# Kernel tuning notes

Measured on AMD Instinct MI355X. Metric: run time of the kernel, lower is better.

## Reference

```python
import jax, jax.numpy as jnp
import numpy as np

B, S, D, H = 2, 2048, 1024, 16
HD = D // H  # head_dim = 64


def setup_inputs() -> dict:
    key = jax.random.key(0)
    ks = jax.random.split(key, 11)
    s = 1.0 / np.sqrt(D)
    return {
        "query": jax.random.normal(ks[0], (B, S, D), jnp.float32),
        "key": jax.random.normal(ks[1], (B, S, D), jnp.float32),
        "value": jax.random.normal(ks[2], (B, S, D), jnp.float32),
        "Wq": jax.random.uniform(ks[3], (D, D), jnp.float32, -s, s),
        "bq": jax.random.uniform(ks[4], (D,), jnp.float32, -s, s),
        "Wk": jax.random.uniform(ks[5], (D, D), jnp.float32, -s, s),
        "bk": jax.random.uniform(ks[6], (D,), jnp.float32, -s, s),
        "Wv": jax.random.uniform(ks[7], (D, D), jnp.float32, -s, s),
        "bv": jax.random.uniform(ks[8], (D,), jnp.float32, -s, s),
        "Wo": jax.random.uniform(ks[9], (D, D), jnp.float32, -s, s),
        "bo": jax.random.uniform(ks[10], (D,), jnp.float32, -s, s),
    }


def reference(query, key, value, Wq, bq, Wk, bk, Wv, bv, Wo, bo):
    # Linear projections (W stored as [in, out])
    q = query @ Wq + bq  # [B,S,D]
    k = key @ Wk + bk
    v = value @ Wv + bv
    # split heads -> [B,H,S,HD]
    q = q.reshape(B, S, H, HD).transpose(0, 2, 1, 3)
    k = k.reshape(B, S, H, HD).transpose(0, 2, 1, 3)
    v = v.reshape(B, S, H, HD).transpose(0, 2, 1, 3)
    scale = 1.0 / jnp.sqrt(jnp.float32(HD))
    scores = jnp.einsum("bhqd,bhkd->bhqk", q, k) * scale  # [B,H,S,S]
    attn = jax.nn.softmax(scores, axis=-1)
    out = jnp.einsum("bhqk,bhkd->bhqd", attn, v)  # [B,H,S,HD]
    out = out.transpose(0, 2, 1, 3).reshape(B, S, D)
    out = out @ Wo + bo
    return out, attn
```

## Files before the change

### kernel.cpp

```cpp
#include <hip/hip_runtime.h>

typedef __bf16 bf16;
typedef __bf16 bf16x8 __attribute__((ext_vector_type(8)));
typedef __bf16 bf16x4 __attribute__((ext_vector_type(4)));
typedef float  f32x4  __attribute__((ext_vector_type(4)));

#define B_ 2
#define S_ 2048
#define D_ 1024
#define H_ 16
#define HD_ 64
#define MROWS_ (B_*S_)

__global__ __launch_bounds__(256) void convert_kernel(
    const float* __restrict__ q, const float* __restrict__ k, const float* __restrict__ v,
    bf16* __restrict__ qx, bf16* __restrict__ kx, bf16* __restrict__ vx)
{
    size_t i = ((size_t)blockIdx.x * 256 + threadIdx.x) * 4;
    float4 a = *(const float4*)(q + i);
    float4 b = *(const float4*)(k + i);
    float4 c = *(const float4*)(v + i);
    bf16x4 oa = { (bf16)a.x, (bf16)a.y, (bf16)a.z, (bf16)a.w };
    bf16x4 ob = { (bf16)b.x, (bf16)b.y, (bf16)b.z, (bf16)b.w };
    bf16x4 oc = { (bf16)c.x, (bf16)c.y, (bf16)c.z, (bf16)c.w };
    *(bf16x4*)(qx + i) = oa;
    *(bf16x4*)(kx + i) = ob;
    *(bf16x4*)(vx + i) = oc;
}

__global__ __launch_bounds__(256) void wtrans_kernel(
    const float* __restrict__ W0, const float* __restrict__ W1,
    const float* __restrict__ W2, const float* __restrict__ W3,
    bf16* __restrict__ T0, bf16* __restrict__ T1,
    bf16* __restrict__ T2, bf16* __restrict__ T3)
{
    int z = blockIdx.z;
    const float* W = z == 0 ? W0 : (z == 1 ? W1 : (z == 2 ? W2 : W3));
    bf16* T = z == 0 ? T0 : (z == 1 ? T1 : (z == 2 ? T2 : T3));
    __shared__ float tile[32][33];
    int n0 = blockIdx.x * 32, k0 = blockIdx.y * 32;
    int tx = threadIdx.x, ty = threadIdx.y;
#pragma unroll
    for (int r = 0; r < 4; r++)
        tile[ty + r * 8][tx] = W[(size_t)(k0 + ty + r * 8) * D_ + n0 + tx];
    __syncthreads();
#pragma unroll
    for (int r = 0; r < 4; r++)
        T[(size_t)(n0 + ty + r * 8) * D_ + k0 + tx] = (bf16)tile[tx][ty + r * 8];
}

template <int OUT_MODE>
__global__ __launch_bounds__(256) void gemm_bias_kernel(
    const bf16* __restrict__ A0, const bf16* __restrict__ A1, const bf16* __restrict__ A2,
    const bf16* __restrict__ B0, const bf16* __restrict__ B1, const bf16* __restrict__ B2,
    const float* __restrict__ bias0, const float* __restrict__ bias1, const float* __restrict__ bias2,
    void* __restrict__ out0, void* __restrict__ out1, void* __restrict__ out2)
{
    constexpr int K = 1024, N = 1024;
    int z = blockIdx.z;
    const bf16* A = z == 0 ? A0 : (z == 1 ? A1 : A2);
    const bf16* Bt = z == 0 ? B0 : (z == 1 ? B1 : B2);
    const float* bias = z == 0 ? bias0 : (z == 1 ? bias1 : bias2);
    void* out = z == 0 ? out0 : (z == 1 ? out1 : out2);

    __shared__ bf16 sA[128][40];
    __shared__ bf16 sB[128][40];

    int tid = threadIdx.x, wave = tid >> 6, lane = tid & 63;
    int lrow = lane & 15, quad = lane >> 4;
    int m0 = blockIdx.y * 128, n0 = blockIdx.x * 128;
    int rb = (wave & 1) * 64, cb = (wave >> 1) * 64;

    f32x4 acc[4][4] = {};

    for (int k0 = 0; k0 < K; k0 += 32) {
        __syncthreads();
#pragma unroll
        for (int it = 0; it < 2; it++) {
            int idx = tid + it * 256;
            int r = idx >> 2, c = (idx & 3) * 8;
            *(uint4*)&sA[r][c] = *(const uint4*)(A + (size_t)(m0 + r) * K + k0 + c);
            *(uint4*)&sB[r][c] = *(const uint4*)(Bt + (size_t)(n0 + r) * K + k0 + c);
        }
        __syncthreads();
        bf16x8 af[4], bfv[4];
#pragma unroll
        for (int t = 0; t < 4; t++) {
            af[t]  = *(const bf16x8*)&sA[rb + t * 16 + lrow][quad * 8];
            bfv[t] = *(const bf16x8*)&sB[cb + t * 16 + lrow][quad * 8];
        }
#pragma unroll
        for (int rt = 0; rt < 4; rt++)
#pragma unroll
            for (int ct = 0; ct < 4; ct++)
                acc[rt][ct] = __builtin_amdgcn_mfma_f32_16x16x32_bf16(af[rt], bfv[ct], acc[rt][ct], 0, 0, 0);
    }

#pragma unroll
    for (int ct = 0; ct < 4; ct++) {
        int n = n0 + cb + ct * 16 + lrow;
        float bv = bias[n];
#pragma unroll
        for (int rt = 0; rt < 4; rt++) {
            int m = m0 + rb + rt * 16 + quad * 4;
#pragma unroll
            for (int rr = 0; rr < 4; rr++) {
                float val = acc[rt][ct][rr] + bv;
                if (OUT_MODE == 0) ((bf16*)out)[(size_t)(m + rr) * N + n] = (bf16)val;
                else               ((float*)out)[(size_t)(m + rr) * N + n] = val;
            }
        }
    }
}

__global__ __launch_bounds__(256) void vtrans_kernel(
    const bf16* __restrict__ vp, bf16* __restrict__ vT)
{
    __shared__ bf16 tile[64][72];
    int s0 = blockIdx.x * 64;
    int bh = blockIdx.y;
    int b = bh >> 4, h = bh & 15;
    int tid = threadIdx.x;
#pragma unroll
    for (int it = 0; it < 2; it++) {
        int idx = tid + it * 256;
        int s = idx >> 3, c = (idx & 7) * 8;
        *(uint4*)&tile[s][c] = *(const uint4*)&vp[(size_t)(b * S_ + s0 + s) * D_ + h * HD_ + c];
    }
    __syncthreads();
#pragma unroll
    for (int it = 0; it < 2; it++) {
        int idx = tid + it * 256;
        int d = idx >> 3, c = (idx & 7) * 8;
        bf16x8 t;
#pragma unroll
        for (int j = 0; j < 8; j++) t[j] = tile[c + j][d];
        *(bf16x8*)&vT[(size_t)(bh * HD_ + d) * S_ + s0 + c] = t;
    }
}

__global__ __launch_bounds__(256) void attn_kernel(
    const bf16* __restrict__ qp, const bf16* __restrict__ kp, const bf16* __restrict__ vT,
    float* __restrict__ attn, bf16* __restrict__ op)
{
    __shared__ bf16 sQ[64][72];
    __shared__ bf16 sK[128][72];
    __shared__ bf16 sVT[64][136];
    __shared__ bf16 sP[64][136];
    __shared__ float sInv[64];

    int qt = blockIdx.x, bh = blockIdx.y;
    int b = bh >> 4, h = bh & 15;
    int q0 = qt * 64;
    int tid = threadIdx.x, wave = tid >> 6, lane = tid & 63;
    int lrow = lane & 15, quad = lane >> 4;
    const float scale = 0.125f;

    const size_t qbase = (size_t)(b * S_ + q0) * D_ + h * HD_;
#pragma unroll
    for (int it = 0; it < 2; it++) {
        int idx = tid + it * 256;
        int r = idx >> 3, c = (idx & 7) * 8;
        *(uint4*)&sQ[r][c] = *(const uint4*)&qp[qbase + (size_t)r * D_ + c];
    }
    __syncthreads();
    bf16x8 aq0 = *(const bf16x8*)&sQ[wave * 16 + lrow][quad * 8];
    bf16x8 aq1 = *(const bf16x8*)&sQ[wave * 16 + lrow][32 + quad * 8];

    const size_t kbase0 = (size_t)(b * S_) * D_ + h * HD_;

    float rsum[4] = {0.f, 0.f, 0.f, 0.f};
    for (int kt = 0; kt < 16; kt++) {
        __syncthreads();
#pragma unroll
        for (int it = 0; it < 4; it++) {
            int idx = tid + it * 256;
            int r = idx >> 3, c = (idx & 7) * 8;
            *(uint4*)&sK[r][c] = *(const uint4*)&kp[kbase0 + (size_t)(kt * 128 + r) * D_ + c];
        }
        __syncthreads();
#pragma unroll
        for (int ct = 0; ct < 8; ct++) {
            f32x4 s = {0.f, 0.f, 0.f, 0.f};
            bf16x8 b0 = *(const bf16x8*)&sK[ct * 16 + lrow][quad * 8];
            bf16x8 b1 = *(const bf16x8*)&sK[ct * 16 + lrow][32 + quad * 8];
            s = __builtin_amdgcn_mfma_f32_16x16x32_bf16(aq0, b0, s, 0, 0, 0);
            s = __builtin_amdgcn_mfma_f32_16x16x32_bf16(aq1, b1, s, 0, 0, 0);
#pragma unroll
            for (int r = 0; r < 4; r++) rsum[r] += __expf(s[r] * scale);
        }
    }
#pragma unroll
    for (int off = 1; off < 16; off <<= 1)
#pragma unroll
        for (int r = 0; r < 4; r++) rsum[r] += __shfl_xor(rsum[r], off);
    if (lrow == 0) {
#pragma unroll
        for (int r = 0; r < 4; r++) sInv[wave * 16 + quad * 4 + r] = 1.0f / rsum[r];
    }
    __syncthreads();
    float inv[4];
#pragma unroll
    for (int r = 0; r < 4; r++) inv[r] = sInv[wave * 16 + quad * 4 + r];

    f32x4 oacc[4] = {};
    float* attn_base = attn + ((size_t)bh * S_ + q0) * S_;
    const size_t vbase = (size_t)(bh * HD_) * S_;
    for (int kt = 0; kt < 16; kt++) {
        __syncthreads();
#pragma unroll
        for (int it = 0; it < 4; it++) {
            int idx = tid + it * 256;
            int r = idx >> 3, c = (idx & 7) * 8;
            *(uint4*)&sK[r][c] = *(const uint4*)&kp[kbase0 + (size_t)(kt * 128 + r) * D_ + c];
        }
#pragma unroll
        for (int it = 0; it < 4; it++) {
            int idx = tid + it * 256;
            int d = idx >> 4, c = (idx & 15) * 8;
            *(uint4*)&sVT[d][c] = *(const uint4*)&vT[vbase + (size_t)d * S_ + kt * 128 + c];
        }
        __syncthreads();
#pragma unroll
        for (int ct = 0; ct < 8; ct++) {
            f32x4 s = {0.f, 0.f, 0.f, 0.f};
            bf16x8 b0 = *(const bf16x8*)&sK[ct * 16 + lrow][quad * 8];
            bf16x8 b1 = *(const bf16x8*)&sK[ct * 16 + lrow][32 + quad * 8];
            s = __builtin_amdgcn_mfma_f32_16x16x32_bf16(aq0, b0, s, 0, 0, 0);
            s = __builtin_amdgcn_mfma_f32_16x16x32_bf16(aq1, b1, s, 0, 0, 0);
            int key_local = ct * 16 + lrow;
#pragma unroll
            for (int r = 0; r < 4; r++) {
                float e = __expf(s[r] * scale) * inv[r];
                int qrow = wave * 16 + quad * 4 + r;
                attn_base[(size_t)qrow * S_ + kt * 128 + key_local] = e;
                sP[qrow][key_local] = (bf16)e;
            }
        }
        bf16x8 ap[4];
#pragma unroll
        for (int ks = 0; ks < 4; ks++)
            ap[ks] = *(const bf16x8*)&sP[wave * 16 + lrow][ks * 32 + quad * 8];
#pragma unroll
        for (int dt = 0; dt < 4; dt++)
#pragma unroll
            for (int ks = 0; ks < 4; ks++) {
                bf16x8 bv = *(const bf16x8*)&sVT[dt * 16 + lrow][ks * 32 + quad * 8];
                oacc[dt] = __builtin_amdgcn_mfma_f32_16x16x32_bf16(ap[ks], bv, oacc[dt], 0, 0, 0);
            }
    }

#pragma unroll
    for (int dt = 0; dt < 4; dt++)
#pragma unroll
        for (int r = 0; r < 4; r++) {
            int qrow = q0 + wave * 16 + quad * 4 + r;
            op[(size_t)(b * S_ + qrow) * D_ + h * HD_ + dt * 16 + lrow] = (bf16)oacc[dt][r];
        }
}

extern "C" void kernel_launch(void* const* d_in, const int* in_sizes, int n_in,
                              void* d_out, int out_size, void* d_ws, size_t ws_size,
                              hipStream_t stream)
{
    const float* query = (const float*)d_in[0];
    const float* key_  = (const float*)d_in[1];
    const float* value = (const float*)d_in[2];
    const float* Wq = (const float*)d_in[3];
    const float* bq = (const float*)d_in[4];
    const float* Wk = (const float*)d_in[5];
    const float* bk = (const float*)d_in[6];
    const float* Wv = (const float*)d_in[7];
    const float* bv = (const float*)d_in[8];
    const float* Wo = (const float*)d_in[9];
    const float* bo = (const float*)d_in[10];

    float* out  = (float*)d_out;
    float* attn = out + (size_t)B_ * S_ * D_;

    char* ws = (char*)d_ws;
    const size_t SZ_BSD = (size_t)MROWS_ * D_ * sizeof(bf16);
    const size_t SZ_W   = (size_t)D_ * D_ * sizeof(bf16);
    bf16* qx  = (bf16*)(ws + 0 * SZ_BSD);
    bf16* kx  = (bf16*)(ws + 1 * SZ_BSD);
    bf16* vx  = (bf16*)(ws + 2 * SZ_BSD);
    bf16* wqT = (bf16*)(ws + 3 * SZ_BSD + 0 * SZ_W);
    bf16* wkT = (bf16*)(ws + 3 * SZ_BSD + 1 * SZ_W);
    bf16* wvT = (bf16*)(ws + 3 * SZ_BSD + 2 * SZ_W);
    bf16* woT = (bf16*)(ws + 3 * SZ_BSD + 3 * SZ_W);
    bf16* qp  = (bf16*)(ws + 3 * SZ_BSD + 4 * SZ_W);
    bf16* kp  = (bf16*)(ws + 4 * SZ_BSD + 4 * SZ_W);
    bf16* vp  = (bf16*)(ws + 5 * SZ_BSD + 4 * SZ_W);
    bf16* vTr = (bf16*)(ws + 0 * SZ_BSD);
    bf16* op  = (bf16*)(ws + 1 * SZ_BSD);

    convert_kernel<<<4096, 256, 0, stream>>>(query, key_, value, qx, kx, vx);
    wtrans_kernel<<<dim3(32, 32, 4), dim3(32, 8), 0, stream>>>(Wq, Wk, Wv, Wo, wqT, wkT, wvT, woT);
    gemm_bias_kernel<0><<<dim3(8, 32, 3), 256, 0, stream>>>(
        qx, kx, vx, wqT, wkT, wvT, bq, bk, bv, qp, kp, vp);
    vtrans_kernel<<<dim3(32, 32), 256, 0, stream>>>(vp, vTr);
    attn_kernel<<<dim3(32, 32), 256, 0, stream>>>(qp, kp, vTr, attn, op);
    gemm_bias_kernel<1><<<dim3(8, 32, 1), 256, 0, stream>>>(
        op, op, op, woT, woT, woT, bo, bo, bo, out, out, out);
}
```

Before: 772.8 us.

## Restructure attention to 128-row tiles with direct-register K/V loads and XCD-aware mapping

The attention kernel now gives each block 128 query rows (32 per wave) and loads K and V^T fragments straight from global memory into registers instead of staging them through LDS. It also maps blocks so that each XCD works on the same heads, folds the softmax scale into the Q projection epilogue, and writes the attention matrix and final output with nontemporal stores. The GEMM loads its tiles with global_load_lds direct-to-LDS copies into an unpadded layout. These changes target LDS traffic, barriers and L2 locality. The costs are more global loads with poorer coalescing, possible LDS bank conflicts in the unpadded GEMM tiles, and half as many attention blocks.

```diff
diff --git a/kernel.cpp b/kernel.cpp
--- a/kernel.cpp
+++ b/kernel.cpp
@@ -11,6 +11,12 @@
 #define H_ 16
 #define HD_ 64
 #define MROWS_ (B_*S_)
+
+__device__ __forceinline__ void gld_lds16(const bf16* g, bf16* l) {
+    __builtin_amdgcn_global_load_lds(
+        (const __attribute__((address_space(1))) void*)g,
+        (__attribute__((address_space(3))) void*)l, 16, 0, 0);
+}
 
 __global__ __launch_bounds__(256) void convert_kernel(
     const float* __restrict__ q, const float* __restrict__ k, const float* __restrict__ v,
@@ -49,7 +55,7 @@
         T[(size_t)(n0 + ty + r * 8) * D_ + k0 + tx] = (bf16)tile[tx][ty + r * 8];
 }
 
-template <int OUT_MODE>
+template <int OUT_MODE, int SCALE_Z0>
 __global__ __launch_bounds__(256) void gemm_bias_kernel(
     const bf16* __restrict__ A0, const bf16* __restrict__ A1, const bf16* __restrict__ A2,
     const bf16* __restrict__ B0, const bf16* __restrict__ B1, const bf16* __restrict__ B2,
@@ -63,8 +69,8 @@
     const float* bias = z == 0 ? bias0 : (z == 1 ? bias1 : bias2);
     void* out = z == 0 ? out0 : (z == 1 ? out1 : out2);
 
-    __shared__ bf16 sA[128][40];
-    __shared__ bf16 sB[128][40];
+    __shared__ bf16 sA[128 * 32];
+    __shared__ bf16 sB[128 * 32];
 
     int tid = threadIdx.x, wave = tid >> 6, lane = tid & 63;
     int lrow = lane & 15, quad = lane >> 4;
@@ -77,17 +83,19 @@
         __syncthreads();
 #pragma unroll
         for (int it = 0; it < 2; it++) {
-            int idx = tid + it * 256;
-            int r = idx >> 2, c = (idx & 3) * 8;
-            *(uint4*)&sA[r][c] = *(const uint4*)(A + (size_t)(m0 + r) * K + k0 + c);
-            *(uint4*)&sB[r][c] = *(const uint4*)(Bt + (size_t)(n0 + r) * K + k0 + c);
+            int chunk = wave * 64 + lane + it * 256;
+            int r = chunk >> 2, c = (chunk & 3) * 8;
+            bf16* la = sA + (size_t)(wave * 64 + it * 256) * 8;
+            bf16* lb = sB + (size_t)(wave * 64 + it * 256) * 8;
+            gld_lds16(A  + (size_t)(m0 + r) * K + k0 + c, la);
+            gld_lds16(Bt + (size_t)(n0 + r) * K + k0 + c, lb);
         }
         __syncthreads();
         bf16x8 af[4], bfv[4];
 #pragma unroll
         for (int t = 0; t < 4; t++) {
-            af[t]  = *(const bf16x8*)&sA[rb + t * 16 + lrow][quad * 8];
-            bfv[t] = *(const bf16x8*)&sB[cb + t * 16 + lrow][quad * 8];
+            af[t]  = *(const bf16x8*)&sA[(rb + t * 16 + lrow) * 32 + quad * 8];
+            bfv[t] = *(const bf16x8*)&sB[(cb + t * 16 + lrow) * 32 + quad * 8];
         }
 #pragma unroll
         for (int rt = 0; rt < 4; rt++)
@@ -106,8 +114,9 @@
 #pragma unroll
             for (int rr = 0; rr < 4; rr++) {
                 float val = acc[rt][ct][rr] + bv;
+                if (SCALE_Z0 && z == 0) val *= 0.125f;
                 if (OUT_MODE == 0) ((bf16*)out)[(size_t)(m + rr) * N + n] = (bf16)val;
-                else               ((float*)out)[(size_t)(m + rr) * N + n] = val;
+                else __builtin_nontemporal_store(val, &((float*)out)[(size_t)(m + rr) * N + n]);
             }
         }
     }
@@ -143,120 +152,119 @@
     const bf16* __restrict__ qp, const bf16* __restrict__ kp, const bf16* __restrict__ vT,
     float* __restrict__ attn, bf16* __restrict__ op)
 {
-    __shared__ bf16 sQ[64][72];
-    __shared__ bf16 sK[128][72];
-    __shared__ bf16 sVT[64][136];
-    __shared__ bf16 sP[64][136];
-    __shared__ float sInv[64];
-
-    int qt = blockIdx.x, bh = blockIdx.y;
+    __shared__ bf16 sP[128][136];
+
+    int bid = blockIdx.x;
+    int xcd = bid & 7, idx = bid >> 3;
+    int bh = xcd + 8 * (idx >> 4);
+    int qt = idx & 15;
     int b = bh >> 4, h = bh & 15;
-    int q0 = qt * 64;
+    int q0 = qt * 128;
+
     int tid = threadIdx.x, wave = tid >> 6, lane = tid & 63;
     int lrow = lane & 15, quad = lane >> 4;
-    const float scale = 0.125f;
-
-    const size_t qbase = (size_t)(b * S_ + q0) * D_ + h * HD_;
-#pragma unroll
-    for (int it = 0; it < 2; it++) {
-        int idx = tid + it * 256;
-        int r = idx >> 3, c = (idx & 7) * 8;
-        *(uint4*)&sQ[r][c] = *(const uint4*)&qp[qbase + (size_t)r * D_ + c];
-    }
-    __syncthreads();
-    bf16x8 aq0 = *(const bf16x8*)&sQ[wave * 16 + lrow][quad * 8];
-    bf16x8 aq1 = *(const bf16x8*)&sQ[wave * 16 + lrow][32 + quad * 8];
-
-    const size_t kbase0 = (size_t)(b * S_) * D_ + h * HD_;
-
-    float rsum[4] = {0.f, 0.f, 0.f, 0.f};
+
+    bf16x8 aq[2][2];
+#pragma unroll
+    for (int sb = 0; sb < 2; sb++) {
+        const bf16* qr = qp + (size_t)(b * S_ + q0 + wave * 32 + sb * 16 + lrow) * D_ + h * HD_ + quad * 8;
+        aq[sb][0] = *(const bf16x8*)qr;
+        aq[sb][1] = *(const bf16x8*)(qr + 32);
+    }
+
+    const bf16* kbase = kp + (size_t)(b * S_) * D_ + h * HD_ + quad * 8;
+
+    float rsum[2][4] = {};
     for (int kt = 0; kt < 16; kt++) {
-        __syncthreads();
-#pragma unroll
-        for (int it = 0; it < 4; it++) {
-            int idx = tid + it * 256;
-            int r = idx >> 3, c = (idx & 7) * 8;
-            *(uint4*)&sK[r][c] = *(const uint4*)&kp[kbase0 + (size_t)(kt * 128 + r) * D_ + c];
-        }
-        __syncthreads();
-#pragma unroll
-        for (int ct = 0; ct < 8; ct++) {
-            f32x4 s = {0.f, 0.f, 0.f, 0.f};
-            bf16x8 b0 = *(const bf16x8*)&sK[ct * 16 + lrow][quad * 8];
-            bf16x8 b1 = *(const bf16x8*)&sK[ct * 16 + lrow][32 + quad * 8];
-            s = __builtin_amdgcn_mfma_f32_16x16x32_bf16(aq0, b0, s, 0, 0, 0);
-            s = __builtin_amdgcn_mfma_f32_16x16x32_bf16(aq1, b1, s, 0, 0, 0);
-#pragma unroll
-            for (int r = 0; r < 4; r++) rsum[r] += __expf(s[r] * scale);
+#pragma unroll
+        for (int hf = 0; hf < 2; hf++) {
+            bf16x8 kb0[4], kb1[4];
+#pragma unroll
+            for (int c = 0; c < 4; c++) {
+                const bf16* kr = kbase + (size_t)(kt * 128 + hf * 64 + c * 16 + lrow) * D_;
+                kb0[c] = *(const bf16x8*)kr;
+                kb1[c] = *(const bf16x8*)(kr + 32);
+            }
+#pragma unroll
+            for (int c = 0; c < 4; c++)
+#pragma unroll
+                for (int sb = 0; sb < 2; sb++) {
+                    f32x4 s = {0.f, 0.f, 0.f, 0.f};
+                    s = __builtin_amdgcn_mfma_f32_16x16x32_bf16(aq[sb][0], kb0[c], s, 0, 0, 0);
+                    s = __builtin_amdgcn_mfma_f32_16x16x32_bf16(aq[sb][1], kb1[c], s, 0, 0, 0);
+#pragma unroll
+                    for (int r = 0; r < 4; r++) rsum[sb][r] += __expf(s[r]);
+                }
         }
     }
 #pragma unroll
     for (int off = 1; off < 16; off <<= 1)
 #pragma unroll
-        for (int r = 0; r < 4; r++) rsum[r] += __shfl_xor(rsum[r], off);
-    if (lrow == 0) {
-#pragma unroll
-        for (int r = 0; r < 4; r++) sInv[wave * 16 + quad * 4 + r] = 1.0f / rsum[r];
-    }
-    __syncthreads();
-    float inv[4];
-#pragma unroll
-    for (int r = 0; r < 4; r++) inv[r] = sInv[wave * 16 + quad * 4 + r];
-
-    f32x4 oacc[4] = {};
+        for (int sb = 0; sb < 2; sb++)
+#pragma unroll
+            for (int r = 0; r < 4; r++) rsum[sb][r] += __shfl_xor(rsum[sb][r], off);
+    float inv[2][4];
+#pragma unroll
+    for (int sb = 0; sb < 2; sb++)
+#pragma unroll
+        for (int r = 0; r < 4; r++) inv[sb][r] = 1.0f / rsum[sb][r];
+
+    f32x4 oacc[2][4] = {};
     float* attn_base = attn + ((size_t)bh * S_ + q0) * S_;
-    const size_t vbase = (size_t)(bh * HD_) * S_;
+    const bf16* vbase = vT + (size_t)bh * HD_ * S_;
     for (int kt = 0; kt < 16; kt++) {
-        __syncthreads();
-#pragma unroll
-        for (int it = 0; it < 4; it++) {
-            int idx = tid + it * 256;
-            int r = idx >> 3, c = (idx & 7) * 8;
-            *(uint4*)&sK[r][c] = *(const uint4*)&kp[kbase0 + (size_t)(kt * 128 + r) * D_ + c];
-        }
-#pragma unroll
-        for (int it = 0; it < 4; it++) {
-            int idx = tid + it * 256;
-            int d = idx >> 4, c = (idx & 15) * 8;
-            *(uint4*)&sVT[d][c] = *(const uint4*)&vT[vbase + (size_t)d * S_ + kt * 128 + c];
-        }
-        __syncthreads();
-#pragma unroll
-        for (int ct = 0; ct < 8; ct++) {
-            f32x4 s = {0.f, 0.f, 0.f, 0.f};
-            bf16x8 b0 = *(const bf16x8*)&sK[ct * 16 + lrow][quad * 8];
-            bf16x8 b1 = *(const bf16x8*)&sK[ct * 16 + lrow][32 + quad * 8];
-            s = __builtin_amdgcn_mfma_f32_16x16x32_bf16(aq0, b0, s, 0, 0, 0);
-            s = __builtin_amdgcn_mfma_f32_16x16x32_bf16(aq1, b1, s, 0, 0, 0);
-            int key_local = ct * 16 + lrow;
+#pragma unroll
+        for (int hf = 0; hf < 2; hf++) {
+            bf16x8 kb0[4], kb1[4];
+#pragma unroll
+            for (int c = 0; c < 4; c++) {
+                const bf16* kr = kbase + (size_t)(kt * 128 + hf * 64 + c * 16 + lrow) * D_;
+                kb0[c] = *(const bf16x8*)kr;
+                kb1[c] = *(const bf16x8*)(kr + 32);
+            }
+#pragma unroll
+            for (int c = 0; c < 4; c++)
+#pragma unroll
+                for (int sb = 0; sb < 2; sb++) {
+                    f32x4 s = {0.f, 0.f, 0.f, 0.f};
+                    s = __builtin_amdgcn_mfma_f32_16x16x32_bf16(aq[sb][0], kb0[c], s, 0, 0, 0);
+                    s = __builtin_amdgcn_mfma_f32_16x16x32_bf16(aq[sb][1], kb1[c], s, 0, 0, 0);
+                    int key = hf * 64 + c * 16 + lrow;
+#pragma unroll
+                    for (int r = 0; r < 4; r++) {
+                        float e = __expf(s[r]) * inv[sb][r];
+                        int qrl = wave * 32 + sb * 16 + quad * 4 + r;
+                        __builtin_nontemporal_store(e, attn_base + (size_t)qrl * S_ + kt * 128 + key);
+                        sP[qrl][key] = (bf16)e;
+                    }
+                }
+        }
+        bf16x8 ap[2][4];
+#pragma unroll
+        for (int sb = 0; sb < 2; sb++)
+#pragma unroll
+            for (int ks = 0; ks < 4; ks++)
+                ap[sb][ks] = *(const bf16x8*)&sP[wave * 32 + sb * 16 + lrow][ks * 32 + quad * 8];
+#pragma unroll
+        for (int dt = 0; dt < 4; dt++)
+#pragma unroll
+            for (int ks = 0; ks < 4; ks++) {
+                bf16x8 vb = *(const bf16x8*)&vbase[(size_t)(dt * 16 + lrow) * S_ + kt * 128 + ks * 32 + quad * 8];
+#pragma unroll
+                for (int sb = 0; sb < 2; sb++)
+                    oacc[sb][dt] = __builtin_amdgcn_mfma_f32_16x16x32_bf16(ap[sb][ks], vb, oacc[sb][dt], 0, 0, 0);
+            }
+    }
+
+#pragma unroll
+    for (int sb = 0; sb < 2; sb++)
+#pragma unroll
+        for (int dt = 0; dt < 4; dt++)
 #pragma unroll
             for (int r = 0; r < 4; r++) {
-                float e = __expf(s[r] * scale) * inv[r];
-                int qrow = wave * 16 + quad * 4 + r;
-                attn_base[(size_t)qrow * S_ + kt * 128 + key_local] = e;
-                sP[qrow][key_local] = (bf16)e;
-            }
-        }
-        bf16x8 ap[4];
-#pragma unroll
-        for (int ks = 0; ks < 4; ks++)
-            ap[ks] = *(const bf16x8*)&sP[wave * 16 + lrow][ks * 32 + quad * 8];
-#pragma unroll
-        for (int dt = 0; dt < 4; dt++)
-#pragma unroll
-            for (int ks = 0; ks < 4; ks++) {
-                bf16x8 bv = *(const bf16x8*)&sVT[dt * 16 + lrow][ks * 32 + quad * 8];
-                oacc[dt] = __builtin_amdgcn_mfma_f32_16x16x32_bf16(ap[ks], bv, oacc[dt], 0, 0, 0);
-            }
-    }
-
-#pragma unroll
-    for (int dt = 0; dt < 4; dt++)
-#pragma unroll
-        for (int r = 0; r < 4; r++) {
-            int qrow = q0 + wave * 16 + quad * 4 + r;
-            op[(size_t)(b * S_ + qrow) * D_ + h * HD_ + dt * 16 + lrow] = (bf16)oacc[dt][r];
-        }
+                int qrow = q0 + wave * 32 + sb * 16 + quad * 4 + r;
+                op[(size_t)(b * S_ + qrow) * D_ + h * HD_ + dt * 16 + lrow] = (bf16)oacc[sb][dt][r];
+            }
 }
 
 extern "C" void kernel_launch(void* const* d_in, const int* in_sizes, int n_in,
@@ -296,10 +304,10 @@
 
     convert_kernel<<<4096, 256, 0, stream>>>(query, key_, value, qx, kx, vx);
     wtrans_kernel<<<dim3(32, 32, 4), dim3(32, 8), 0, stream>>>(Wq, Wk, Wv, Wo, wqT, wkT, wvT, woT);
-    gemm_bias_kernel<0><<<dim3(8, 32, 3), 256, 0, stream>>>(
+    gemm_bias_kernel<0, 1><<<dim3(8, 32, 3), 256, 0, stream>>>(
         qx, kx, vx, wqT, wkT, wvT, bq, bk, bv, qp, kp, vp);
     vtrans_kernel<<<dim3(32, 32), 256, 0, stream>>>(vp, vTr);
-    attn_kernel<<<dim3(32, 32), 256, 0, stream>>>(qp, kp, vTr, attn, op);
-    gemm_bias_kernel<1><<<dim3(8, 32, 1), 256, 0, stream>>>(
+    attn_kernel<<<512, 256, 0, stream>>>(qp, kp, vTr, attn, op);
+    gemm_bias_kernel<1, 0><<<dim3(8, 32, 1), 256, 0, stream>>>(
         op, op, op, woT, woT, woT, bo, bo, bo, out, out, out);
 }
```

New measurement: 871.6 us. 12.8% more time.

## Use direct global-to-LDS loads, fold softmax scale into Q, nontemporal stores, XCD remap

Applied to the files above, without the earlier changes.

The GEMM tile loads now use global_load_lds to copy straight into unpadded LDS, bypassing registers. The 1/sqrt(d) scale is folded into the Q projection epilogue, which removes the per-score multiply in attention. The attention-probability and output stores become nontemporal, and the attention grid is flattened with an XCD-aware block remap so blocks of the same head share a die's L2. Unpadded LDS rows may cause bank conflicts on fragment reads, and scaling before bf16 rounding slightly changes numerics.

```diff
diff --git a/kernel.cpp b/kernel.cpp
--- a/kernel.cpp
+++ b/kernel.cpp
@@ -11,6 +11,12 @@
 #define H_ 16
 #define HD_ 64
 #define MROWS_ (B_*S_)
+
+__device__ __forceinline__ void gld_lds16(const bf16* g, bf16* l) {
+    __builtin_amdgcn_global_load_lds(
+        (const __attribute__((address_space(1))) void*)g,
+        (__attribute__((address_space(3))) void*)l, 16, 0, 0);
+}
 
 __global__ __launch_bounds__(256) void convert_kernel(
     const float* __restrict__ q, const float* __restrict__ k, const float* __restrict__ v,
@@ -49,7 +55,7 @@
         T[(size_t)(n0 + ty + r * 8) * D_ + k0 + tx] = (bf16)tile[tx][ty + r * 8];
 }
 
-template <int OUT_MODE>
+template <int OUT_MODE, int SCALE_Z0>
 __global__ __launch_bounds__(256) void gemm_bias_kernel(
     const bf16* __restrict__ A0, const bf16* __restrict__ A1, const bf16* __restrict__ A2,
     const bf16* __restrict__ B0, const bf16* __restrict__ B1, const bf16* __restrict__ B2,
@@ -63,8 +69,8 @@
     const float* bias = z == 0 ? bias0 : (z == 1 ? bias1 : bias2);
     void* out = z == 0 ? out0 : (z == 1 ? out1 : out2);
 
-    __shared__ bf16 sA[128][40];
-    __shared__ bf16 sB[128][40];
+    __shared__ bf16 sA[128 * 32];
+    __shared__ bf16 sB[128 * 32];
 
     int tid = threadIdx.x, wave = tid >> 6, lane = tid & 63;
     int lrow = lane & 15, quad = lane >> 4;
@@ -77,17 +83,19 @@
         __syncthreads();
 #pragma unroll
         for (int it = 0; it < 2; it++) {
-            int idx = tid + it * 256;
-            int r = idx >> 2, c = (idx & 3) * 8;
-            *(uint4*)&sA[r][c] = *(const uint4*)(A + (size_t)(m0 + r) * K + k0 + c);
-            *(uint4*)&sB[r][c] = *(const uint4*)(Bt + (size_t)(n0 + r) * K + k0 + c);
+            int chunk = wave * 64 + lane + it * 256;
+            int r = chunk >> 2, c = (chunk & 3) * 8;
+            bf16* la = sA + (size_t)(wave * 64 + it * 256) * 8;
+            bf16* lb = sB + (size_t)(wave * 64 + it * 256) * 8;
+            gld_lds16(A  + (size_t)(m0 + r) * K + k0 + c, la);
+            gld_lds16(Bt + (size_t)(n0 + r) * K + k0 + c, lb);
         }
         __syncthreads();
         bf16x8 af[4], bfv[4];
 #pragma unroll
         for (int t = 0; t < 4; t++) {
-            af[t]  = *(const bf16x8*)&sA[rb + t * 16 + lrow][quad * 8];
-            bfv[t] = *(const bf16x8*)&sB[cb + t * 16 + lrow][quad * 8];
+            af[t]  = *(const bf16x8*)&sA[(rb + t * 16 + lrow) * 32 + quad * 8];
+            bfv[t] = *(const bf16x8*)&sB[(cb + t * 16 + lrow) * 32 + quad * 8];
         }
 #pragma unroll
         for (int rt = 0; rt < 4; rt++)
@@ -106,8 +114,9 @@
 #pragma unroll
             for (int rr = 0; rr < 4; rr++) {
                 float val = acc[rt][ct][rr] + bv;
+                if (SCALE_Z0 && z == 0) val *= 0.125f;
                 if (OUT_MODE == 0) ((bf16*)out)[(size_t)(m + rr) * N + n] = (bf16)val;
-                else               ((float*)out)[(size_t)(m + rr) * N + n] = val;
+                else __builtin_nontemporal_store(val, &((float*)out)[(size_t)(m + rr) * N + n]);
             }
         }
     }
@@ -149,18 +158,20 @@
     __shared__ bf16 sP[64][136];
     __shared__ float sInv[64];
 
-    int qt = blockIdx.x, bh = blockIdx.y;
+    int bid = blockIdx.x;
+    int xcd = bid & 7, idx = bid >> 3;
+    int bh = xcd + 8 * (idx >> 5);
+    int qt = idx & 31;
     int b = bh >> 4, h = bh & 15;
     int q0 = qt * 64;
     int tid = threadIdx.x, wave = tid >> 6, lane = tid & 63;
     int lrow = lane & 15, quad = lane >> 4;
-    const float scale = 0.125f;
 
     const size_t qbase = (size_t)(b * S_ + q0) * D_ + h * HD_;
 #pragma unroll
     for (int it = 0; it < 2; it++) {
-        int idx = tid + it * 256;
-        int r = idx >> 3, c = (idx & 7) * 8;
+        int idx2 = tid + it * 256;
+        int r = idx2 >> 3, c = (idx2 & 7) * 8;
         *(uint4*)&sQ[r][c] = *(const uint4*)&qp[qbase + (size_t)r * D_ + c];
     }
     __syncthreads();
@@ -174,8 +185,8 @@
         __syncthreads();
 #pragma unroll
         for (int it = 0; it < 4; it++) {
-            int idx = tid + it * 256;
-            int r = idx >> 3, c = (idx & 7) * 8;
+            int idx2 = tid + it * 256;
+            int r = idx2 >> 3, c = (idx2 & 7) * 8;
             *(uint4*)&sK[r][c] = *(const uint4*)&kp[kbase0 + (size_t)(kt * 128 + r) * D_ + c];
         }
         __syncthreads();
@@ -187,7 +198,7 @@
             s = __builtin_amdgcn_mfma_f32_16x16x32_bf16(aq0, b0, s, 0, 0, 0);
             s = __builtin_amdgcn_mfma_f32_16x16x32_bf16(aq1, b1, s, 0, 0, 0);
 #pragma unroll
-            for (int r = 0; r < 4; r++) rsum[r] += __expf(s[r] * scale);
+            for (int r = 0; r < 4; r++) rsum[r] += __expf(s[r]);
         }
     }
 #pragma unroll
@@ -210,14 +221,14 @@
         __syncthreads();
 #pragma unroll
         for (int it = 0; it < 4; it++) {
-            int idx = tid + it * 256;
-            int r = idx >> 3, c = (idx & 7) * 8;
+            int idx2 = tid + it * 256;
+            int r = idx2 >> 3, c = (idx2 & 7) * 8;
             *(uint4*)&sK[r][c] = *(const uint4*)&kp[kbase0 + (size_t)(kt * 128 + r) * D_ + c];
         }
 #pragma unroll
         for (int it = 0; it < 4; it++) {
-            int idx = tid + it * 256;
-            int d = idx >> 4, c = (idx & 15) * 8;
+            int idx2 = tid + it * 256;
+            int d = idx2 >> 4, c = (idx2 & 15) * 8;
             *(uint4*)&sVT[d][c] = *(const uint4*)&vT[vbase + (size_t)d * S_ + kt * 128 + c];
         }
         __syncthreads();
@@ -231,9 +242,9 @@
             int key_local = ct * 16 + lrow;
 #pragma unroll
             for (int r = 0; r < 4; r++) {
-                float e = __expf(s[r] * scale) * inv[r];
+                float e = __expf(s[r]) * inv[r];
                 int qrow = wave * 16 + quad * 4 + r;
-                attn_base[(size_t)qrow * S_ + kt * 128 + key_local] = e;
+                __builtin_nontemporal_store(e, attn_base + (size_t)qrow * S_ + kt * 128 + key_local);
                 sP[qrow][key_local] = (bf16)e;
             }
         }
@@ -296,10 +307,10 @@
 
     convert_kernel<<<4096, 256, 0, stream>>>(query, key_, value, qx, kx, vx);
     wtrans_kernel<<<dim3(32, 32, 4), dim3(32, 8), 0, stream>>>(Wq, Wk, Wv, Wo, wqT, wkT, wvT, woT);
-    gemm_bias_kernel<0><<<dim3(8, 32, 3), 256, 0, stream>>>(
+    gemm_bias_kernel<0, 1><<<dim3(8, 32, 3), 256, 0, stream>>>(
         qx, kx, vx, wqT, wkT, wvT, bq, bk, bv, qp, kp, vp);
     vtrans_kernel<<<dim3(32, 32), 256, 0, stream>>>(vp, vTr);
-    attn_kernel<<<dim3(32, 32), 256, 0, stream>>>(qp, kp, vTr, attn, op);
-    gemm_bias_kernel<1><<<dim3(8, 32, 1), 256, 0, stream>>>(
+    attn_kernel<<<1024, 256, 0, stream>>>(qp, kp, vTr, attn, op);
+    gemm_bias_kernel<1, 0><<<dim3(8, 32, 1), 256, 0, stream>>>(
         op, op, op, woT, woT, woT, bo, bo, bo, out, out, out);
 }
```

New measurement: 745.9 us. 1.04x faster.
